# Kernel tuning notes

Hardware: AMD Instinct MI355X
Metric: run time of the kernel (lower is better)

## Reference

```python
import jax, jax.numpy as jnp
from jax import lax
import numpy as np

M, CLS, K, DL, DC, DO, BD = 87, 65, 128, 128, 128, 2048, 256
B, H, W = 256, 7, 7


def _c1(x, Wt, b):
    # 1x1 Conv2d: [B,Cin,H,W] -> [B,Cout,H,W]
    return jnp.einsum('oc,bchw->bohw', Wt, x) + b[None, :, None, None]


def _pagerank(edge, v_init, p=0.85, iters=100):
    # torch: transition = adj / adj.sum(dim=1)  (broadcast divides COLUMNS by row-sums)
    n = edge.shape[0]
    Wpr = p * edge / jnp.sum(edge, axis=1)[None, :]
    s = v_init * n                                  # [B,n,1]
    coef = (1.0 - p) / n
    def body(i, xv):
        zx = coef * jnp.sum(xv, axis=1, keepdims=True)      # z_T @ x -> [B,1,1]
        return jnp.einsum('ij,bjo->bio', Wpr, xv) + s * zx
    xv = lax.fori_loop(0, iters, body, s)
    nrm = jnp.sqrt(jnp.sum(xv * xv, axis=1, keepdims=True))  # F.normalize(dim=1)
    xv = xv / jnp.maximum(nrm, 1e-12)
    return (v_init + xv).reshape(v_init.shape[0], -1)        # [B,n]


def setup_inputs() -> dict:
    key = jax.random.key(0)
    ks = jax.random.split(key, 24)
    def w(k, shape, s=0.02):
        return jax.random.normal(k, shape, jnp.float32) * s
    rng = np.random.default_rng(0)
    A = (rng.random((M, M)) < 0.08).astype(np.float32)
    A = np.maximum(A, A.T)
    np.fill_diagonal(A, 1.0)   # symmetric adjacency with self-loops (degrees > 0)
    return {
        'x': jax.random.normal(ks[0], (B, DO, H, W), jnp.float32),
        'Wb': w(ks[1], (BD, DO)), 'bb': w(ks[2], (BD,), 0.01),
        'Wfc': w(ks[3], (CLS, BD)), 'Wfc2': w(ks[4], (CLS, BD)),
        'Wo1': w(ks[5], (4 * DL, DO)), 'bo1': w(ks[6], (4 * DL,), 0.01),
        'Wo2': w(ks[7], (DL, 4 * DL)), 'bo2': w(ks[8], (DL,), 0.01),
        'Wa': w(ks[9], (M, DL)), 'ba': w(ks[10], (M,), 0.01),
        'Wps': w(ks[11], (DC, DL)), 'bps': w(ks[12], (DC,), 0.01),
        'node_p': jax.random.uniform(ks[13], (K, M), jnp.float32, -0.1, 0.1),
        'Wg': w(ks[14], (DC, DC + K)), 'bg': w(ks[15], (DC,), 0.01),
        'Wsp': w(ks[16], (DL, DC)), 'bsp': w(ks[17], (DL,), 0.01),
        'Ws': w(ks[18], (1, DC + DL)), 'bs': w(ks[19], (1,), 0.01),
        'Wox1': w(ks[20], (4 * DL, DL)), 'box1': w(ks[21], (4 * DL,), 0.01),
        'Wox2': w(ks[22], (DO, 4 * DL)), 'box2': w(ks[23], (DO,), 0.01),
        'edge': jnp.asarray(A),
    }


def reference(x, Wb, bb, Wfc, Wfc2, Wo1, bo1, Wo2, bo2, Wa, ba, Wps, bps,
              node_p, Wg, bg, Wsp, bsp, Ws, bs, Wox1, box1, Wox2, box2, edge):
    Bsz, _, hl, wl = x.shape
    HW = hl * wl

    # global pooled branch
    x_p = jnp.mean(x, axis=(2, 3))                           # [B,2048]
    features_p = x_p @ Wb.T + bb                             # [B,256]
    pre_output = features_p @ Wfc.T                          # [B,65]
    pre_score = jax.nn.softmax(lax.stop_gradient(pre_output), axis=1)

    # personalized pagerank over the semantic graph (constant wrt grads)
    v_init = jnp.concatenate(
        [jnp.zeros((Bsz, M - CLS), x.dtype), pre_score], axis=1)[:, :, None]
    v_y = lax.stop_gradient(_pagerank(edge, v_init))         # [B,87]

    # local feature reduction 2048 -> 512 -> 128
    x_l = _c1(_c1(x, Wo1, bo1), Wo2, bo2)                    # [B,128,7,7]

    a = _c1(x_l, Wa, ba).reshape(Bsz, M, HW).transpose(0, 2, 1)   # [B,HW,87]
    ps = _c1(x_l, Wps, bps).reshape(Bsz, DC, HW)                  # [B,128,HW]
    m1 = jax.nn.relu(jnp.matmul(ps, a))                           # [B,128,87]

    # replicate torch's exact (k, B*m) reshape + flat v_y broadcast
    node = jnp.broadcast_to(node_p[None], (Bsz, K, M)).reshape(K, Bsz * M)
    node = (v_y.reshape(-1) * node).reshape(Bsz, K, M)

    g = jnp.einsum('oc,bcm->bom', Wg, jnp.concatenate([node, m1], axis=1)) \
        + bg[None, :, None]                                   # [B,128,87]

    # D^-1/2 A D^-1/2 graph propagation
    Dinv = jnp.sum(edge, axis=0) ** -0.5
    edge_norm = Dinv[:, None] * edge * Dinv[None, :]
    m2 = jax.nn.relu(jnp.einsum('bcm,mn->bcn', g, edge_norm))  # [B,128,87]

    sp = jnp.einsum('oc,bcm->bom', Wsp, m2) + bsp[None, :, None]  # [B,128,87]

    # conv_s over concat(m2_expand, x_expand) is separable: avoid the
    # [B,256,HW,87] tensor entirely (1 output channel, 1x1 kernel).
    Ws1, Ws2 = Ws[0, :DC], Ws[0, DC:]
    t_node = jnp.einsum('c,bcm->bm', Ws1, m2)                  # [B,87]
    t_pix = jnp.einsum('c,bcp->bp', Ws2, x_l.reshape(Bsz, DL, HW))  # [B,HW]
    s_logits = t_node[:, :, None] + t_pix[:, None, :] + bs[0]  # [B,87,HW]
    s_att = jax.nn.softmax(s_logits, axis=1)                   # softmax over nodes

    m3 = jax.nn.relu(jnp.matmul(sp, s_att)).reshape(Bsz, DL, hl, wl)
    m3 = _c1(_c1(m3, Wox1, box1), Wox2, box2)                  # [B,2048,7,7]

    feature_aug = jnp.mean(m3, axis=(2, 3)) @ Wb.T + bb
    features = features_p + feature_aug
    outputs2 = features @ Wfc2.T
    softmax_outputs = jax.nn.softmax(outputs2, axis=1)
    return (features, outputs2, softmax_outputs, pre_output, features_p)
```

## Files before the change

kernel.cpp:

```cpp
#include <hip/hip_runtime.h>
#include <cmath>


typedef __attribute__((ext_vector_type(8))) short short8;
typedef __attribute__((ext_vector_type(4))) short s16x4;
typedef __attribute__((ext_vector_type(4))) float f32x4;

constexpr size_t OFF_W12BF = 0;
constexpr size_t OFF_T1BF  = 131072;
constexpr size_t OFF_WBBF  = 262144;
constexpr size_t OFF_XPBF  = 524288;
constexpr size_t OFF_WAPBF = 786432;
constexpr size_t OFF_WG2BF = 800768;
constexpr size_t OFF_ENPBF = 808960;
constexpr size_t OFF_B215  = 813568;
constexpr size_t OFF_B12   = 813792;
constexpr size_t OFF_WPR   = 813920;
constexpr size_t OFF_BTMP  = 821496;
constexpr size_t OFF_WC    = 823544;
constexpr size_t OFF_BC    = 856312;
constexpr size_t OFF_VY    = 856568;
constexpr size_t OFF_NT    = 878848;
constexpr size_t OFF_PART  = 901376;

__device__ __forceinline__ unsigned short f2bf(float f) {
  unsigned u = __builtin_bit_cast(unsigned, f);
  u += 0x7fffu + ((u >> 16) & 1u);
  return (unsigned short)(u >> 16);
}
__device__ __forceinline__ float bf2f(unsigned short s) {
  return __builtin_bit_cast(float, ((unsigned)s) << 16);
}

__global__ __launch_bounds__(256) void ksetup_all(
    const float* __restrict__ Wb,  const float* __restrict__ bb,
    const float* __restrict__ Wa,  const float* __restrict__ ba,
    const float* __restrict__ Wps, const float* __restrict__ bps,
    const float* __restrict__ Wg,  const float* __restrict__ edge,
    const float* __restrict__ Wo2, const float* __restrict__ Wo1,
    const float* __restrict__ Wox2,const float* __restrict__ Wox1,
    const float* __restrict__ box1,const float* __restrict__ box2,
    const float* __restrict__ bo1, const float* __restrict__ bo2,
    float* __restrict__ ws, float* __restrict__ featp)
{
  __shared__ alignas(16) short As[64*72];
  __shared__ alignas(16) short Bs[64*72];
  int blk = blockIdx.x, tid = threadIdx.x;
  if (blk < 256) {
    int base = (blk*256 + tid)*8;
    float4 v0 = *(const float4*)&Wb[base];
    float4 v1 = *(const float4*)&Wb[base+4];
    short8 sv;
    sv[0]=(short)f2bf(v0.x); sv[1]=(short)f2bf(v0.y); sv[2]=(short)f2bf(v0.z); sv[3]=(short)f2bf(v0.w);
    sv[4]=(short)f2bf(v1.x); sv[5]=(short)f2bf(v1.y); sv[6]=(short)f2bf(v1.z); sv[7]=(short)f2bf(v1.w);
    *(short8*)&((unsigned short*)(ws+OFF_WBBF))[base] = sv;
  } else if (blk < 320) {
    int idx4 = ((blk-256)*256 + tid)*4;
    float4 bv = *(const float4*)&bb[idx4 & 255];
    *(float4*)&featp[idx4] = bv;
  } else if (blk < 352) {
    int idx4 = ((blk-320)*256 + tid)*4;
    float4 z; z.x=z.y=z.z=z.w=0.f;
    *(float4*)&ws[OFF_WC + idx4] = z;
  } else if (blk < 380) {
    int idx4 = ((blk-352)*256 + tid)*4;
    int r = idx4 >> 7, c = idx4 & 127;
    float4 v;
    if (r < 128)      v = *(const float4*)&Wps[r*128 + c];
    else if (r < 215) v = *(const float4*)&Wa[(r-128)*128 + c];
    else              { v.x=v.y=v.z=v.w=0.f; }
    s16x4 sv; sv[0]=(short)f2bf(v.x); sv[1]=(short)f2bf(v.y); sv[2]=(short)f2bf(v.z); sv[3]=(short)f2bf(v.w);
    *(s16x4*)&((unsigned short*)(ws+OFF_WAPBF))[idx4] = sv;
  } else if (blk < 396) {
    int idx4 = ((blk-380)*256 + tid)*4;
    int o = idx4 >> 7, d = idx4 & 127;
    float4 v = *(const float4*)&Wg[o*256 + 128 + d];
    s16x4 sv; sv[0]=(short)f2bf(v.x); sv[1]=(short)f2bf(v.y); sv[2]=(short)f2bf(v.z); sv[3]=(short)f2bf(v.w);
    *(s16x4*)&((unsigned short*)(ws+OFF_WG2BF))[idx4] = sv;
  } else if (blk < 432) {
    int idx = (blk-396)*256 + tid;
    int m = idx / 96, n = idx % 96;
    float v = 0.f;
    if (m < 87 && n < 87) {
      float sm = 0.f, sn = 0.f;
      for (int k = 0; k < 87; ++k) { sm += edge[k*87+m]; sn += edge[k*87+n]; }
      v = edge[m*87+n] / sqrtf(sm*sn);
    }
    ((unsigned short*)(ws+OFF_ENPBF))[idx] = f2bf(v);
  } else if (blk < 462) {
    int idx = (blk-432)*256 + tid;
    if (idx < 87*87) {
      int j = idx % 87;
      float rs = 0.f;
      for (int k = 0; k < 87; ++k) rs += edge[j*87+k];
      ws[OFF_WPR + idx] = 0.85f * edge[idx] / rs;
    }
  } else if (blk == 462) {
    if (tid < 224) {
      float v = (tid < 128) ? bps[tid] : (tid < 215 ? ba[tid-128] : 0.f);
      ws[OFF_B215 + tid] = v;
    }
  } else if (blk < 591) {
    int gb = blk - 463;
    const float *A, *B; unsigned short* C; int lda, ldb, ldc, i0, j0;
    if (gb < 64) {
      A = Wo2; B = Wo1; C = (unsigned short*)(ws+OFF_W12BF);
      lda = 512; ldb = 2048; ldc = 2048;
      i0 = (gb & 1)*64; j0 = (gb >> 1)*64;
    } else {
      int b2 = gb - 64;
      A = Wox2; B = Wox1; C = (unsigned short*)(ws+OFF_T1BF);
      lda = 512; ldb = 128; ldc = 128;
      i0 = (b2 >> 1)*64; j0 = (b2 & 1)*64;
    }
    int w = tid >> 6, l = tid & 63, quad = l >> 4, lane16 = l & 15;
    f32x4 acc[4];
    #pragma unroll
    for (int i = 0; i < 4; ++i) acc[i] = (f32x4)(0.f);
    for (int kc = 0; kc < 512; kc += 64) {
      for (int t = tid; t < 1024; t += 256) {
        int r = t >> 4, k4 = t & 15;
        float4 v = *(const float4*)&A[(size_t)(i0+r)*lda + kc + k4*4];
        s16x4 sv; sv[0]=(short)f2bf(v.x); sv[1]=(short)f2bf(v.y); sv[2]=(short)f2bf(v.z); sv[3]=(short)f2bf(v.w);
        *(s16x4*)&As[r*72 + k4*4] = sv;
      }
      for (int t = tid; t < 1024; t += 256) {
        int kr = t >> 4, n4 = t & 15;
        float4 v = *(const float4*)&B[(size_t)(kc+kr)*ldb + j0 + n4*4];
        Bs[(n4*4+0)*72 + kr] = (short)f2bf(v.x);
        Bs[(n4*4+1)*72 + kr] = (short)f2bf(v.y);
        Bs[(n4*4+2)*72 + kr] = (short)f2bf(v.z);
        Bs[(n4*4+3)*72 + kr] = (short)f2bf(v.w);
      }
      __syncthreads();
      #pragma unroll
      for (int ks = 0; ks < 2; ++ks) {
        short8 a = *(const short8*)&As[(w*16+lane16)*72 + ks*32 + quad*8];
        #pragma unroll
        for (int nt = 0; nt < 4; ++nt) {
          short8 b8 = *(const short8*)&Bs[(nt*16+lane16)*72 + ks*32 + quad*8];
          acc[nt] = __builtin_amdgcn_mfma_f32_16x16x32_bf16(a, b8, acc[nt], 0, 0, 0);
        }
      }
      __syncthreads();
    }
    #pragma unroll
    for (int nt = 0; nt < 4; ++nt)
      #pragma unroll
      for (int r = 0; r < 4; ++r)
        C[(size_t)(i0 + w*16 + quad*4 + r)*ldc + j0 + nt*16 + lane16] = f2bf(acc[nt][r]);
  } else {
    int vb = blk - 591;
    int w = tid >> 6, l = tid & 63;
    if (vb < 512) {
      int o = vb*4 + w;
      float s = 0.f;
      for (int h = l; h < 512; h += 64) s += Wox2[(size_t)o*512 + h] * box1[h];
      for (int off = 32; off; off >>= 1) s += __shfl_down(s, off, 64);
      if (l == 0) ws[OFF_BTMP + o] = s + box2[o];
    } else {
      int o = (vb - 512)*4 + w;
      float s = 0.f;
      for (int h = l; h < 512; h += 64) s += Wo2[(size_t)o*512 + h] * bo1[h];
      for (int off = 32; off; off >>= 1) s += __shfl_down(s, off, 64);
      if (l == 0) ws[OFF_B12 + o] = s + bo2[o];
    }
  }
}

__global__ __launch_bounds__(512, 4) void kmain5(const float* __restrict__ x,
                                                 const short* __restrict__ w12bf,
                                                 short* __restrict__ xpbf,
                                                 float* __restrict__ part)
{
  __shared__ alignas(16) short Bt[2][64*72];
  __shared__ alignas(16) float xpp[2][832];
  int b = blockIdx.x, q = blockIdx.y, tid = threadIdx.x;
  int w = tid >> 6, l = tid & 63;
  int quad = l >> 4, lane16 = l & 15;
  const float* xb = x + ((size_t)b*2048 + q*1024)*49;

  int p4A = tid % 13, cA = tid / 13;
  int tB = tid + 512;
  int p4B = tB % 13, cB = tB / 13;
  bool hasB = (tid < 320);

  float fA[4], fB[4];
  {
    if (p4A < 12) {
      float4 v = *(const float4*)(xb + cA*49 + p4A*4);
      fA[0]=v.x; fA[1]=v.y; fA[2]=v.z; fA[3]=v.w;
    } else fA[0] = xb[cA*49 + 48];
    if (hasB) {
      if (p4B < 12) {
        float4 v = *(const float4*)(xb + cB*49 + p4B*4);
        fB[0]=v.x; fB[1]=v.y; fB[2]=v.z; fB[3]=v.w;
      } else fB[0] = xb[cB*49 + 48];
    }
  }

  f32x4 acc[4];
  #pragma unroll
  for (int i = 0; i < 4; ++i) acc[i] = (f32x4)(0.f);

  for (int kci = 0; kci < 16; ++kci) {
    short* bt = Bt[kci & 1];
    float* xp = xpp[kci & 1];
    if (p4A < 12) {
      #pragma unroll
      for (int i = 0; i < 4; ++i) bt[(p4A*4+i)*72 + cA] = (short)f2bf(fA[i]);
      xp[tid] = fA[0]+fA[1]+fA[2]+fA[3];
    } else {
      bt[48*72 + cA] = (short)f2bf(fA[0]);
      xp[tid] = fA[0];
    }
    if (hasB) {
      if (p4B < 12) {
        #pragma unroll
        for (int i = 0; i < 4; ++i) bt[(p4B*4+i)*72 + cB] = (short)f2bf(fB[i]);
        xp[512 + tid] = fB[0]+fB[1]+fB[2]+fB[3];
      } else {
        bt[48*72 + cB] = (short)f2bf(fB[0]);
        xp[512 + tid] = fB[0];
      }
    }
    __syncthreads();
    if (kci < 15) {
      const float* xc = xb + (size_t)(kci+1)*64*49;
      if (p4A < 12) {
        float4 v = *(const float4*)(xc + cA*49 + p4A*4);
        fA[0]=v.x; fA[1]=v.y; fA[2]=v.z; fA[3]=v.w;
      } else fA[0] = xc[cA*49 + 48];
      if (hasB) {
        if (p4B < 12) {
          float4 v = *(const float4*)(xc + cB*49 + p4B*4);
          fB[0]=v.x; fB[1]=v.y; fB[2]=v.z; fB[3]=v.w;
        } else fB[0] = xc[cB*49 + 48];
      }
    }
    const short* wr = w12bf + (size_t)(w*16 + lane16)*2048 + q*1024 + kci*64 + quad*8;
    short8 a0 = *(const short8*)(wr);
    short8 a1 = *(const short8*)(wr + 32);
    #pragma unroll
    for (int ni = 0; ni < 4; ++ni) {
      const short* br = bt + (ni*16 + lane16)*72 + quad*8;
      short8 b0 = *(const short8*)(br);
      short8 b1 = *(const short8*)(br + 32);
      acc[ni] = __builtin_amdgcn_mfma_f32_16x16x32_bf16(a0, b0, acc[ni], 0, 0, 0);
      acc[ni] = __builtin_amdgcn_mfma_f32_16x16x32_bf16(a1, b1, acc[ni], 0, 0, 0);
    }
    if (tid < 64) {
      float s = 0.f;
      #pragma unroll
      for (int j = 0; j < 13; ++j) s += xp[tid*13 + j];
      xpbf[(size_t)b*2048 + q*1024 + kci*64 + tid] = (short)f2bf(s * (1.f/49.f));
    }
  }
  float* po = part + ((size_t)q*256 + b)*6656;
  #pragma unroll
  for (int ni = 0; ni < 4; ++ni) {
    int p = ni*16 + lane16;
    if (p < 49) {
      #pragma unroll
      for (int r = 0; r < 4; ++r) {
        int o = w*16 + quad*4 + r;
        po[o*52 + p] = acc[ni][r];
      }
    }
  }
}

__global__ __launch_bounds__(256) void kwcf(const float* __restrict__ Wb,
                                            const float* __restrict__ bb,
                                            const short* __restrict__ xpbf,
                                            float* __restrict__ featp,
                                            float* __restrict__ ws)
{
  __shared__ alignas(16) short As[64*72];
  __shared__ alignas(16) short Bs[64*72];
  int blk = blockIdx.x, tid = threadIdx.x;
  if (blk < 64) {
    const short* wbbf = (const short*)(ws+OFF_WBBF);
    const short* t1s  = (const short*)(ws+OFF_T1BF);
    int i0 = (blk & 3)*64, j0 = ((blk >> 2) & 1)*64, kc0 = (blk >> 3)*256;
    int w = tid >> 6, l = tid & 63, quad = l >> 4, lane16 = l & 15;
    f32x4 acc[4];
    #pragma unroll
    for (int i = 0; i < 4; ++i) acc[i] = (f32x4)(0.f);
    for (int kc = kc0; kc < kc0+256; kc += 64) {
      for (int t = tid; t < 512; t += 256) {
        int r = t >> 3, c8 = t & 7;
        *(short8*)&As[r*72 + c8*8] = *(const short8*)&wbbf[(size_t)(i0+r)*2048 + kc + c8*8];
      }
      for (int t = tid; t < 1024; t += 256) {
        int kr = t >> 4, n4 = t & 15;
        s16x4 v = *(const s16x4*)&t1s[(size_t)(kc+kr)*128 + j0 + n4*4];
        Bs[(n4*4+0)*72 + kr] = v[0];
        Bs[(n4*4+1)*72 + kr] = v[1];
        Bs[(n4*4+2)*72 + kr] = v[2];
        Bs[(n4*4+3)*72 + kr] = v[3];
      }
      __syncthreads();
      #pragma unroll
      for (int ks = 0; ks < 2; ++ks) {
        short8 a = *(const short8*)&As[(w*16+lane16)*72 + ks*32 + quad*8];
        #pragma unroll
        for (int nt = 0; nt < 4; ++nt) {
          short8 b8 = *(const short8*)&Bs[(nt*16+lane16)*72 + ks*32 + quad*8];
          acc[nt] = __builtin_amdgcn_mfma_f32_16x16x32_bf16(a, b8, acc[nt], 0, 0, 0);
        }
      }
      __syncthreads();
    }
    #pragma unroll
    for (int nt = 0; nt < 4; ++nt)
      #pragma unroll
      for (int r = 0; r < 4; ++r)
        atomicAdd(&ws[OFF_WC + (size_t)(i0 + w*16 + quad*4 + r)*128 + j0 + nt*16 + lane16], acc[nt][r]);
  } else if (blk < 128) {
    int j = (blk-64)*4 + (tid >> 6), l = tid & 63;
    float s = 0.f;
    for (int c = l; c < 2048; c += 64) s += Wb[(size_t)j*2048 + c] * ws[OFF_BTMP + c];
    for (int off = 32; off; off >>= 1) s += __shfl_down(s, off, 64);
    if (l == 0) ws[OFF_BC + j] = s + bb[j];
  } else {
    const short* wbbf = (const short*)(ws+OFF_WBBF);
    int idx = blk - 128;
    int i0 = (idx & 3)*64, j0 = ((idx >> 2) & 3)*64, kc0 = (idx >> 4)*256;
    int w = tid >> 6, l = tid & 63, quad = l >> 4, lane16 = l & 15;
    f32x4 acc[4];
    #pragma unroll
    for (int i = 0; i < 4; ++i) acc[i] = (f32x4)(0.f);
    for (int kc = kc0; kc < kc0+256; kc += 32) {
      short8 a = *(const short8*)&xpbf[(size_t)(i0 + w*16 + lane16)*2048 + kc + quad*8];
      #pragma unroll
      for (int nt = 0; nt < 4; ++nt) {
        short8 b8 = *(const short8*)&wbbf[(size_t)(j0 + nt*16 + lane16)*2048 + kc + quad*8];
        acc[nt] = __builtin_amdgcn_mfma_f32_16x16x32_bf16(a, b8, acc[nt], 0, 0, 0);
      }
    }
    #pragma unroll
    for (int nt = 0; nt < 4; ++nt)
      #pragma unroll
      for (int r = 0; r < 4; ++r)
        atomicAdd(&featp[(size_t)(i0 + w*16 + quad*4 + r)*256 + j0 + nt*16 + lane16], acc[nt][r]);
  }
}

__global__ __launch_bounds__(384) void kpr(const float* __restrict__ featp,
                                           const float* __restrict__ Wfc,
                                           const float* __restrict__ wpr,
                                           float* __restrict__ preo,
                                           float* __restrict__ vy)
{
  __shared__ alignas(16) float fpr[256];
  __shared__ alignas(16) float po[68];
  __shared__ alignas(16) float vsA[88];
  __shared__ alignas(16) float vsB[88];
  __shared__ alignas(16) float vis[88];
  __shared__ float rd[4];
  int b = blockIdx.x, tid = threadIdx.x;
  if (tid < 256) fpr[tid] = featp[b*256 + tid];
  __syncthreads();
  if (tid < 260) {
    int row = tid >> 2, p = tid & 3;
    float s = 0.f;
    const float* wr = Wfc + row*256 + p*64;
    #pragma unroll
    for (int c = 0; c < 64; c += 4) {
      float4 w4 = *(const float4*)&wr[c];
      s += w4.x*fpr[p*64+c] + w4.y*fpr[p*64+c+1] + w4.z*fpr[p*64+c+2] + w4.w*fpr[p*64+c+3];
    }
    s += __shfl_xor(s, 1, 64);
    s += __shfl_xor(s, 2, 64);
    if (p == 0) { po[row] = s; preo[b*65 + row] = s; }
  }
  __syncthreads();
  if (tid < 64) {
    float v = po[tid];
    if (tid == 0) v = fmaxf(v, po[64]);
    float mx = v;
    #pragma unroll
    for (int off = 32; off; off >>= 1) mx = fmaxf(mx, __shfl_down(mx, off, 64));
    mx = __shfl(mx, 0, 64);
    float e = expf(po[tid]-mx) + ((tid == 0) ? expf(po[64]-mx) : 0.f);
    float sm = e;
    #pragma unroll
    for (int off = 32; off; off >>= 1) sm += __shfl_down(sm, off, 64);
    if (tid == 0) { rd[0] = mx; rd[1] = 1.f/sm; }
  }
  __syncthreads();
  if (tid < 88) {
    float vin = (tid >= 22 && tid < 87) ? expf(po[tid-22]-rd[0])*rd[1] : 0.f;
    vis[tid] = vin;
    vsA[tid] = vin * 87.f;
    vsB[tid] = 0.f;
  }
  __syncthreads();
  float wrow[22];
  const int m4 = tid >> 2, pp = tid & 3;
  if (tid < 348) {
    float add = vis[m4] * 0.15f;
    #pragma unroll
    for (int jj = 0; jj < 22; ++jj) {
      int j = pp*22 + jj;
      wrow[jj] = (j < 87) ? (wpr[m4*87 + j] + add) : 0.f;
    }
  }
  for (int it = 0; it < 64; ++it) {
    const float* vc = (it & 1) ? vsB : vsA;
    float* vn = (it & 1) ? vsA : vsB;
    if (tid < 348) {
      float nv = 0.f;
      #pragma unroll
      for (int jj = 0; jj < 22; ++jj) nv += wrow[jj] * vc[pp*22 + jj];
      nv += __shfl_xor(nv, 1, 64);
      nv += __shfl_xor(nv, 2, 64);
      if (pp == 0) vn[m4] = nv;
    }
    __syncthreads();
  }
  if (tid < 64) {
    float v = vsA[tid]*vsA[tid];
    if (tid < 23) v += vsA[64+tid]*vsA[64+tid];
    #pragma unroll
    for (int off = 32; off; off >>= 1) v += __shfl_down(v, off, 64);
    if (tid == 0) rd[2] = 1.f / fmaxf(sqrtf(v), 1e-12f);
  }
  __syncthreads();
  if (tid < 87) vy[b*87 + tid] = vis[tid] + vsA[tid]*rd[2];
}

__global__ __launch_bounds__(384) void knode(const float* __restrict__ Wg,
                                             const float* __restrict__ node_p,
                                             const float* __restrict__ vy,
                                             float* __restrict__ nt)
{
  int tid = threadIdx.x;
  if (tid >= 352) return;
  int out = blockIdx.x*88 + (tid >> 2);
  int par = out / 11264;
  int r = out % 11264;
  int o = r / 88, m = r % 88;
  int p = tid & 3;
  float s = 0.f;
  if (m < 87) {
    const float* vrow = vy + (size_t)(par*128)*87 + m;
    for (int k = p*32; k < p*32+32; ++k)
      s += Wg[o*256 + k] * node_p[k*87 + m] * vrow[k*87];
  }
  s += __shfl_xor(s, 1, 64);
  s += __shfl_xor(s, 2, 64);
  if (p == 0) nt[out] = s;
}

__global__ __launch_bounds__(512) void kgraph_all(
    const float* __restrict__ part,  const float* __restrict__ b12,
    const short* __restrict__ wapbf, const float* __restrict__ b215,
    const short* __restrict__ wg2bf, const float* __restrict__ nt,
    const float* __restrict__ bg,    const short* __restrict__ enpbf,
    const float* __restrict__ Wsp,   const float* __restrict__ bsp,
    const float* __restrict__ Ws,    const float* __restrict__ wc,
    const float* __restrict__ bc,    const float* __restrict__ featp,
    const float* __restrict__ Wfc2,
    float* __restrict__ feat, float* __restrict__ out2, float* __restrict__ soft)
{
  extern __shared__ char smraw[];
  short* XT = (short*)smraw;
  short* At = XT + 8704;
  short* M1 = At + 16128;
  short* G  = M1 + 13056;
  short* M2 = G  + 13312;
  float* fb  = (float*)(M2 + 13312);
  float* wsm = fb;
  float* tnb = fb + 96;
  float* zs  = fb + 192;
  float* m3s = fb + 320;
  float* fs  = fb + 448;
  float* o2s = fb + 704;
  float* red = fb + 776;

  int b = blockIdx.x, tid = threadIdx.x;
  int w = tid >> 6, l = tid & 63, quad = l >> 4, lane16 = l & 15;

  const float* p0 = part + (size_t)b*6656;
  const float* p1 = p0 + (size_t)256*6656;
  for (int t = tid; t < 6656; t += 512) {
    int o = t / 52, p = t % 52;
    XT[p*136 + o] = (short)f2bf(p0[t] + p1[t] + b12[o]);
  }
  for (int t = tid; t < 1536; t += 512) {
    int p = 52 + t/128, o = t % 128;
    XT[p*136 + o] = 0;
  }
  __syncthreads();

  for (int t = w; t < 56; t += 8) {
    int mt = t >> 2, n4 = t & 3;
    f32x4 acc = (f32x4)(0.f);
    #pragma unroll
    for (int ks = 0; ks < 4; ++ks) {
      short8 a  = *(const short8*)&wapbf[(size_t)(mt*16+lane16)*128 + ks*32 + quad*8];
      short8 b8 = *(const short8*)&XT[(n4*16+lane16)*136 + ks*32 + quad*8];
      acc = __builtin_amdgcn_mfma_f32_16x16x32_bf16(a, b8, acc, 0, 0, 0);
    }
    int p = n4*16 + lane16;
    #pragma unroll
    for (int r = 0; r < 4; ++r) {
      int rr = mt*16 + quad*4 + r;
      At[rr*72 + p] = (p < 49) ? (short)f2bf(acc[r] + b215[rr]) : (short)0;
    }
  }
  __syncthreads();

  for (int t = w; t < 48; t += 8) {
    int mt = t / 8, n4 = t % 8;
    f32x4 acc = (f32x4)(0.f);
    #pragma unroll
    for (int ks = 0; ks < 2; ++ks) {
      short8 a  = *(const short8*)&At[(128 + mt*16 + lane16)*72 + ks*32 + quad*8];
      short8 b8 = *(const short8*)&At[(n4*16+lane16)*72 + ks*32 + quad*8];
      acc = __builtin_amdgcn_mfma_f32_16x16x32_bf16(a, b8, acc, 0, 0, 0);
    }
    int d = n4*16 + lane16;
    #pragma unroll
    for (int r = 0; r < 4; ++r) {
      int m = mt*16 + quad*4 + r;
      M1[m*136 + d] = (short)f2bf(fmaxf(acc[r], 0.f));
    }
  }
  __syncthreads();

  const float* ntb = nt + (size_t)(b & 1)*11264;
  for (int t = w; t < 48; t += 8) {
    int mt = t / 6, n4 = t % 6;
    f32x4 acc = (f32x4)(0.f);
    #pragma unroll
    for (int ks = 0; ks < 4; ++ks) {
      short8 a  = *(const short8*)&wg2bf[(size_t)(mt*16+lane16)*128 + ks*32 + quad*8];
      short8 b8 = *(const short8*)&M1[(n4*16+lane16)*136 + ks*32 + quad*8];
      acc = __builtin_amdgcn_mfma_f32_16x16x32_bf16(a, b8, acc, 0, 0, 0);
    }
    int m = n4*16 + lane16;
    #pragma unroll
    for (int r = 0; r < 4; ++r) {
      int o = mt*16 + quad*4 + r;
      float v = acc[r] + bg[o] + ((m < 88) ? ntb[o*88 + m] : 0.f);
      G[o*104 + m] = (short)f2bf(v);
    }
  }
  __syncthreads();

  for (int t = w; t < 48; t += 8) {
    int mt = t / 6, n4 = t % 6;
    f32x4 acc = (f32x4)(0.f);
    #pragma unroll
    for (int ks = 0; ks < 3; ++ks) {
      short8 a  = *(const short8*)&G[(mt*16+lane16)*104 + ks*32 + quad*8];
      short8 b8 = *(const short8*)&enpbf[(size_t)(n4*16+lane16)*96 + ks*32 + quad*8];
      acc = __builtin_amdgcn_mfma_f32_16x16x32_bf16(a, b8, acc, 0, 0, 0);
    }
    int n = n4*16 + lane16;
    #pragma unroll
    for (int r = 0; r < 4; ++r) {
      int c = mt*16 + quad*4 + r;
      M2[c*104 + n] = (short)f2bf(fmaxf(acc[r], 0.f));
    }
  }
  __syncthreads();

  if (tid < 348) {
    int m = tid >> 2, p = tid & 3;
    float s = 0.f;
    for (int c = p*32; c < p*32+32; ++c)
      s += Ws[c] * bf2f((unsigned short)M2[c*104 + m]);
    s += __shfl_xor(s, 1, 64);
    s += __shfl_xor(s, 2, 64);
    if (p == 0) tnb[m] = s;
  }
  __syncthreads();
  if (tid < 64) {
    float v = tnb[tid];
    if (tid < 23) v = fmaxf(v, tnb[64+tid]);
    float mx = v;
    #pragma unroll
    for (int off = 32; off; off >>= 1) mx = fmaxf(mx, __shfl_down(mx, off, 64));
    mx = __shfl(mx, 0, 64);
    float e0 = expf(tnb[tid]-mx);
    float e1 = (tid < 23) ? expf(tnb[64+tid]-mx) : 0.f;
    float sm = e0 + e1;
    #pragma unroll
    for (int off = 32; off; off >>= 1) sm += __shfl_down(sm, off, 64);
    sm = __shfl(sm, 0, 64);
    float inv = 1.f/sm;
    wsm[tid] = e0*inv;
    if (tid < 23) wsm[64+tid] = e1*inv;
  }
  __syncthreads();
  {
    int c = tid >> 2, p = tid & 3;
    float s = 0.f;
    for (int mm = p*22; mm < p*22+22 && mm < 87; ++mm)
      s += bf2f((unsigned short)M2[c*104 + mm]) * wsm[mm];
    s += __shfl_xor(s, 1, 64);
    s += __shfl_xor(s, 2, 64);
    if (p == 0) zs[c] = s;
  }
  __syncthreads();
  {
    int d = tid >> 2, p = tid & 3;
    float s = 0.f;
    for (int c = p*32; c < p*32+32; ++c) s += Wsp[d*128 + c] * zs[c];
    s += __shfl_xor(s, 1, 64);
    s += __shfl_xor(s, 2, 64);
    if (p == 0) m3s[d] = fmaxf(s + bsp[d], 0.f);
  }
  __syncthreads();

  if (tid < 256) {
    float s = 0.f;
    #pragma unroll 4
    for (int d4 = 0; d4 < 32; ++d4) {
      float4 w4 = *(const float4*)&wc[tid*128 + d4*4];
      s += w4.x*m3s[d4*4] + w4.y*m3s[d4*4+1] + w4.z*m3s[d4*4+2] + w4.w*m3s[d4*4+3];
    }
    float f = featp[b*256 + tid] + bc[tid] + s;
    fs[tid] = f;
    feat[b*256 + tid] = f;
  }
  __syncthreads();
  if (tid < 260) {
    int row = tid >> 2, p = tid & 3;
    float s = 0.f;
    for (int c = p*64; c < p*64+64; c += 4) {
      float4 w4 = *(const float4*)&Wfc2[row*256 + c];
      s += w4.x*fs[c] + w4.y*fs[c+1] + w4.z*fs[c+2] + w4.w*fs[c+3];
    }
    s += __shfl_xor(s, 1, 64);
    s += __shfl_xor(s, 2, 64);
    if (p == 0) { out2[b*65 + row] = s; o2s[row] = s; }
  }
  __syncthreads();
  if (tid < 64) {
    float v = o2s[tid];
    if (tid == 0) v = fmaxf(v, o2s[64]);
    float mx = v;
    #pragma unroll
    for (int off = 32; off; off >>= 1) mx = fmaxf(mx, __shfl_down(mx, off, 64));
    mx = __shfl(mx, 0, 64);
    float e = expf(o2s[tid]-mx) + ((tid == 0) ? expf(o2s[64]-mx) : 0.f);
    float sm = e;
    #pragma unroll
    for (int off = 32; off; off >>= 1) sm += __shfl_down(sm, off, 64);
    if (tid == 0) { red[0] = mx; red[1] = 1.f/sm; }
  }
  __syncthreads();
  if (tid < 65) soft[b*65 + tid] = expf(o2s[tid]-red[0]) * red[1];
}

extern "C" void kernel_launch(void* const* d_in, const int* in_sizes, int n_in,
                              void* d_out, int out_size, void* d_ws, size_t ws_size,
                              hipStream_t stream)
{
  (void)in_sizes; (void)n_in; (void)out_size; (void)ws_size;
  const float* x      = (const float*)d_in[0];
  const float* Wb     = (const float*)d_in[1];
  const float* bb     = (const float*)d_in[2];
  const float* Wfc    = (const float*)d_in[3];
  const float* Wfc2   = (const float*)d_in[4];
  const float* Wo1    = (const float*)d_in[5];
  const float* bo1    = (const float*)d_in[6];
  const float* Wo2    = (const float*)d_in[7];
  const float* bo2    = (const float*)d_in[8];
  const float* Wa     = (const float*)d_in[9];
  const float* ba     = (const float*)d_in[10];
  const float* Wps    = (const float*)d_in[11];
  const float* bps    = (const float*)d_in[12];
  const float* node_p = (const float*)d_in[13];
  const float* Wg     = (const float*)d_in[14];
  const float* bg     = (const float*)d_in[15];
  const float* Wsp    = (const float*)d_in[16];
  const float* bsp    = (const float*)d_in[17];
  const float* Ws     = (const float*)d_in[18];
  const float* Wox1   = (const float*)d_in[20];
  const float* box1   = (const float*)d_in[21];
  const float* Wox2   = (const float*)d_in[22];
  const float* box2   = (const float*)d_in[23];
  const float* edge   = (const float*)d_in[24];

  float* ws   = (float*)d_ws;
  float* out  = (float*)d_out;
  float* feat  = out;
  float* out2  = out + 65536;
  float* soft  = out + 82176;
  float* preo  = out + 98816;
  float* featp = out + 115456;

  ksetup_all<<<1135, 256, 0, stream>>>(Wb, bb, Wa, ba, Wps, bps, Wg, edge,
                                       Wo2, Wo1, Wox2, Wox1, box1, box2, bo1, bo2,
                                       ws, featp);
  kmain5<<<dim3(256,2), 512, 0, stream>>>(x, (const short*)(ws + OFF_W12BF),
                                          (short*)(ws + OFF_XPBF), ws + OFF_PART);
  kwcf<<<256, 256, 0, stream>>>(Wb, bb, (const short*)(ws + OFF_XPBF), featp, ws);
  kpr<<<256, 384, 0, stream>>>(featp, Wfc, ws + OFF_WPR, preo, ws + OFF_VY);
  knode<<<256, 384, 0, stream>>>(Wg, node_p, ws + OFF_VY, ws + OFF_NT);
  kgraph_all<<<256, 512, 132144, stream>>>(ws + OFF_PART, ws + OFF_B12,
                                           (const short*)(ws + OFF_WAPBF),
                                           ws + OFF_B215,
                                           (const short*)(ws + OFF_WG2BF),
                                           ws + OFF_NT, bg,
                                           (const short*)(ws + OFF_ENPBF),
                                           Wsp, bsp, Ws,
                                           ws + OFF_WC, ws + OFF_BC, featp, Wfc2,
                                           feat, out2, soft);
}
```

Measured before the change: 336.7 us.

## Split kmain5 reduction four ways and double-depth prefetch of x chunks

```diff
diff --git a/kernel.cpp b/kernel.cpp
--- a/kernel.cpp
+++ b/kernel.cpp
@@ -168,7 +168,37 @@
   }
 }
 
-__global__ __launch_bounds__(512, 4) void kmain5(const float* __restrict__ x,
+
+#define LOADCH(fR, gR, ptr) do {                                                  \
+    if (p4A < 12) { float4 v_ = *(const float4*)((ptr) + cA*49 + p4A*4);          \
+      fR[0]=v_.x; fR[1]=v_.y; fR[2]=v_.z; fR[3]=v_.w; }                           \
+    else fR[0] = (ptr)[cA*49 + 48];                                               \
+    if (hasB) {                                                                   \
+      if (p4B < 12) { float4 v_ = *(const float4*)((ptr) + cB*49 + p4B*4);        \
+        gR[0]=v_.x; gR[1]=v_.y; gR[2]=v_.z; gR[3]=v_.w; }                         \
+      else gR[0] = (ptr)[cB*49 + 48]; }                                           \
+  } while(0)
+
+#define STAGECH(fR, gR, bt, xp) do {                                              \
+    if (p4A < 12) {                                                               \
+      bt[(p4A*4+0)*72 + cA] = (short)f2bf(fR[0]);                                 \
+      bt[(p4A*4+1)*72 + cA] = (short)f2bf(fR[1]);                                 \
+      bt[(p4A*4+2)*72 + cA] = (short)f2bf(fR[2]);                                 \
+      bt[(p4A*4+3)*72 + cA] = (short)f2bf(fR[3]);                                 \
+      xp[tid] = fR[0]+fR[1]+fR[2]+fR[3];                                          \
+    } else { bt[48*72 + cA] = (short)f2bf(fR[0]); xp[tid] = fR[0]; }              \
+    if (hasB) {                                                                   \
+      if (p4B < 12) {                                                             \
+        bt[(p4B*4+0)*72 + cB] = (short)f2bf(gR[0]);                               \
+        bt[(p4B*4+1)*72 + cB] = (short)f2bf(gR[1]);                               \
+        bt[(p4B*4+2)*72 + cB] = (short)f2bf(gR[2]);                               \
+        bt[(p4B*4+3)*72 + cB] = (short)f2bf(gR[3]);                               \
+        xp[512 + tid] = gR[0]+gR[1]+gR[2]+gR[3];                                  \
+      } else { bt[48*72 + cB] = (short)f2bf(gR[0]); xp[512 + tid] = gR[0]; }      \
+    }                                                                             \
+  } while(0)
+
+__global__ __launch_bounds__(512, 6) void kmain5(const float* __restrict__ x,
                                                  const short* __restrict__ w12bf,
                                                  short* __restrict__ xpbf,
                                                  float* __restrict__ part)
@@ -178,67 +208,34 @@
   int b = blockIdx.x, q = blockIdx.y, tid = threadIdx.x;
   int w = tid >> 6, l = tid & 63;
   int quad = l >> 4, lane16 = l & 15;
-  const float* xb = x + ((size_t)b*2048 + q*1024)*49;
+  const float* xb = x + ((size_t)b*2048 + q*512)*49;
 
   int p4A = tid % 13, cA = tid / 13;
   int tB = tid + 512;
   int p4B = tB % 13, cB = tB / 13;
   bool hasB = (tid < 320);
 
-  float fA[4], fB[4];
-  {
-    if (p4A < 12) {
-      float4 v = *(const float4*)(xb + cA*49 + p4A*4);
-      fA[0]=v.x; fA[1]=v.y; fA[2]=v.z; fA[3]=v.w;
-    } else fA[0] = xb[cA*49 + 48];
-    if (hasB) {
-      if (p4B < 12) {
-        float4 v = *(const float4*)(xb + cB*49 + p4B*4);
-        fB[0]=v.x; fB[1]=v.y; fB[2]=v.z; fB[3]=v.w;
-      } else fB[0] = xb[cB*49 + 48];
-    }
-  }
+  float f0[4], g0[4], f1[4], g1[4];
+  LOADCH(f0, g0, xb);
+  LOADCH(f1, g1, xb + 64*49);
 
   f32x4 acc[4];
   #pragma unroll
   for (int i = 0; i < 4; ++i) acc[i] = (f32x4)(0.f);
 
-  for (int kci = 0; kci < 16; ++kci) {
+  #pragma unroll
+  for (int kci = 0; kci < 8; ++kci) {
     short* bt = Bt[kci & 1];
     float* xp = xpp[kci & 1];
-    if (p4A < 12) {
-      #pragma unroll
-      for (int i = 0; i < 4; ++i) bt[(p4A*4+i)*72 + cA] = (short)f2bf(fA[i]);
-      xp[tid] = fA[0]+fA[1]+fA[2]+fA[3];
-    } else {
-      bt[48*72 + cA] = (short)f2bf(fA[0]);
-      xp[tid] = fA[0];
-    }
-    if (hasB) {
-      if (p4B < 12) {
-        #pragma unroll
-        for (int i = 0; i < 4; ++i) bt[(p4B*4+i)*72 + cB] = (short)f2bf(fB[i]);
-        xp[512 + tid] = fB[0]+fB[1]+fB[2]+fB[3];
-      } else {
-        bt[48*72 + cB] = (short)f2bf(fB[0]);
-        xp[512 + tid] = fB[0];
-      }
-    }
+    if ((kci & 1) == 0) { STAGECH(f0, g0, bt, xp); }
+    else                { STAGECH(f1, g1, bt, xp); }
     __syncthreads();
-    if (kci < 15) {
-      const float* xc = xb + (size_t)(kci+1)*64*49;
-      if (p4A < 12) {
-        float4 v = *(const float4*)(xc + cA*49 + p4A*4);
-        fA[0]=v.x; fA[1]=v.y; fA[2]=v.z; fA[3]=v.w;
-      } else fA[0] = xc[cA*49 + 48];
-      if (hasB) {
-        if (p4B < 12) {
-          float4 v = *(const float4*)(xc + cB*49 + p4B*4);
-          fB[0]=v.x; fB[1]=v.y; fB[2]=v.z; fB[3]=v.w;
-        } else fB[0] = xc[cB*49 + 48];
-      }
-    }
-    const short* wr = w12bf + (size_t)(w*16 + lane16)*2048 + q*1024 + kci*64 + quad*8;
+    if (kci < 6) {
+      const float* xc = xb + (size_t)(kci+2)*64*49;
+      if ((kci & 1) == 0) { LOADCH(f0, g0, xc); }
+      else                { LOADCH(f1, g1, xc); }
+    }
+    const short* wr = w12bf + (size_t)(w*16 + lane16)*2048 + q*512 + kci*64 + quad*8;
     short8 a0 = *(const short8*)(wr);
     short8 a1 = *(const short8*)(wr + 32);
     #pragma unroll
@@ -253,7 +250,7 @@
       float s = 0.f;
       #pragma unroll
       for (int j = 0; j < 13; ++j) s += xp[tid*13 + j];
-      xpbf[(size_t)b*2048 + q*1024 + kci*64 + tid] = (short)f2bf(s * (1.f/49.f));
+      xpbf[(size_t)b*2048 + q*512 + kci*64 + tid] = (short)f2bf(s * (1.f/49.f));
     }
   }
   float* po = part + ((size_t)q*256 + b)*6656;
@@ -485,9 +482,11 @@
 
   const float* p0 = part + (size_t)b*6656;
   const float* p1 = p0 + (size_t)256*6656;
+  const float* p2 = p1 + (size_t)256*6656;
+  const float* p3 = p2 + (size_t)256*6656;
   for (int t = tid; t < 6656; t += 512) {
     int o = t / 52, p = t % 52;
-    XT[p*136 + o] = (short)f2bf(p0[t] + p1[t] + b12[o]);
+    XT[p*136 + o] = (short)f2bf(p0[t] + p1[t] + p2[t] + p3[t] + b12[o]);
   }
   for (int t = tid; t < 1536; t += 512) {
     int p = 52 + t/128, o = t % 128;
@@ -699,7 +698,7 @@
   ksetup_all<<<1135, 256, 0, stream>>>(Wb, bb, Wa, ba, Wps, bps, Wg, edge,
                                        Wo2, Wo1, Wox2, Wox1, box1, box2, bo1, bo2,
                                        ws, featp);
-  kmain5<<<dim3(256,2), 512, 0, stream>>>(x, (const short*)(ws + OFF_W12BF),
+  kmain5<<<dim3(256,4), 512, 0, stream>>>(x, (const short*)(ws + OFF_W12BF),
                                           (short*)(ws + OFF_XPBF), ws + OFF_PART);
   kwcf<<<256, 256, 0, stream>>>(Wb, bb, (const short*)(ws + OFF_XPBF), featp, ws);
   kpr<<<256, 384, 0, stream>>>(featp, Wfc, ws + OFF_WPR, preo, ws + OFF_VY);
```

After: 349.2 us. +3.7%, slower.

## Split main GEMM K four ways and prefetch setup GEMM tiles into registers

Applied to the files above, without the earlier changes.

```diff
diff --git a/kernel.cpp b/kernel.cpp
--- a/kernel.cpp
+++ b/kernel.cpp
@@ -114,25 +114,37 @@
       i0 = (b2 >> 1)*64; j0 = (b2 & 1)*64;
     }
     int w = tid >> 6, l = tid & 63, quad = l >> 4, lane16 = l & 15;
+    int rT[4], c4[4];
+    #pragma unroll
+    for (int j = 0; j < 4; ++j) { int t = tid + j*256; rT[j] = t >> 4; c4[j] = t & 15; }
+    float4 av[4], bv[4];
+    #pragma unroll
+    for (int j = 0; j < 4; ++j) {
+      av[j] = *(const float4*)&A[(size_t)(i0+rT[j])*lda + c4[j]*4];
+      bv[j] = *(const float4*)&B[(size_t)rT[j]*ldb + j0 + c4[j]*4];
+    }
     f32x4 acc[4];
     #pragma unroll
     for (int i = 0; i < 4; ++i) acc[i] = (f32x4)(0.f);
     for (int kc = 0; kc < 512; kc += 64) {
-      for (int t = tid; t < 1024; t += 256) {
-        int r = t >> 4, k4 = t & 15;
-        float4 v = *(const float4*)&A[(size_t)(i0+r)*lda + kc + k4*4];
-        s16x4 sv; sv[0]=(short)f2bf(v.x); sv[1]=(short)f2bf(v.y); sv[2]=(short)f2bf(v.z); sv[3]=(short)f2bf(v.w);
-        *(s16x4*)&As[r*72 + k4*4] = sv;
-      }
-      for (int t = tid; t < 1024; t += 256) {
-        int kr = t >> 4, n4 = t & 15;
-        float4 v = *(const float4*)&B[(size_t)(kc+kr)*ldb + j0 + n4*4];
-        Bs[(n4*4+0)*72 + kr] = (short)f2bf(v.x);
-        Bs[(n4*4+1)*72 + kr] = (short)f2bf(v.y);
-        Bs[(n4*4+2)*72 + kr] = (short)f2bf(v.z);
-        Bs[(n4*4+3)*72 + kr] = (short)f2bf(v.w);
+      #pragma unroll
+      for (int j = 0; j < 4; ++j) {
+        s16x4 sv; sv[0]=(short)f2bf(av[j].x); sv[1]=(short)f2bf(av[j].y);
+        sv[2]=(short)f2bf(av[j].z); sv[3]=(short)f2bf(av[j].w);
+        *(s16x4*)&As[rT[j]*72 + c4[j]*4] = sv;
+        Bs[(c4[j]*4+0)*72 + rT[j]] = (short)f2bf(bv[j].x);
+        Bs[(c4[j]*4+1)*72 + rT[j]] = (short)f2bf(bv[j].y);
+        Bs[(c4[j]*4+2)*72 + rT[j]] = (short)f2bf(bv[j].z);
+        Bs[(c4[j]*4+3)*72 + rT[j]] = (short)f2bf(bv[j].w);
       }
       __syncthreads();
+      if (kc < 448) {
+        #pragma unroll
+        for (int j = 0; j < 4; ++j) {
+          av[j] = *(const float4*)&A[(size_t)(i0+rT[j])*lda + (kc+64) + c4[j]*4];
+          bv[j] = *(const float4*)&B[(size_t)(kc+64+rT[j])*ldb + j0 + c4[j]*4];
+        }
+      }
       #pragma unroll
       for (int ks = 0; ks < 2; ++ks) {
         short8 a = *(const short8*)&As[(w*16+lane16)*72 + ks*32 + quad*8];
@@ -168,17 +180,16 @@
   }
 }
 
-__global__ __launch_bounds__(512, 4) void kmain5(const float* __restrict__ x,
+__global__ __launch_bounds__(512, 6) void kmain5(const float* __restrict__ x,
                                                  const short* __restrict__ w12bf,
                                                  short* __restrict__ xpbf,
                                                  float* __restrict__ part)
 {
   __shared__ alignas(16) short Bt[2][64*72];
-  __shared__ alignas(16) float xpp[2][832];
   int b = blockIdx.x, q = blockIdx.y, tid = threadIdx.x;
   int w = tid >> 6, l = tid & 63;
   int quad = l >> 4, lane16 = l & 15;
-  const float* xb = x + ((size_t)b*2048 + q*1024)*49;
+  const float* xb = x + ((size_t)b*2048 + q*512)*49;
 
   int p4A = tid % 13, cA = tid / 13;
   int tB = tid + 512;
@@ -203,29 +214,20 @@
   #pragma unroll
   for (int i = 0; i < 4; ++i) acc[i] = (f32x4)(0.f);
 
-  for (int kci = 0; kci < 16; ++kci) {
+  for (int kci = 0; kci < 8; ++kci) {
     short* bt = Bt[kci & 1];
-    float* xp = xpp[kci & 1];
     if (p4A < 12) {
       #pragma unroll
       for (int i = 0; i < 4; ++i) bt[(p4A*4+i)*72 + cA] = (short)f2bf(fA[i]);
-      xp[tid] = fA[0]+fA[1]+fA[2]+fA[3];
-    } else {
-      bt[48*72 + cA] = (short)f2bf(fA[0]);
-      xp[tid] = fA[0];
-    }
+    } else bt[48*72 + cA] = (short)f2bf(fA[0]);
     if (hasB) {
       if (p4B < 12) {
         #pragma unroll
         for (int i = 0; i < 4; ++i) bt[(p4B*4+i)*72 + cB] = (short)f2bf(fB[i]);
-        xp[512 + tid] = fB[0]+fB[1]+fB[2]+fB[3];
-      } else {
-        bt[48*72 + cB] = (short)f2bf(fB[0]);
-        xp[512 + tid] = fB[0];
-      }
+      } else bt[48*72 + cB] = (short)f2bf(fB[0]);
     }
     __syncthreads();
-    if (kci < 15) {
+    if (kci < 7) {
       const float* xc = xb + (size_t)(kci+1)*64*49;
       if (p4A < 12) {
         float4 v = *(const float4*)(xc + cA*49 + p4A*4);
@@ -238,7 +240,7 @@
         } else fB[0] = xc[cB*49 + 48];
       }
     }
-    const short* wr = w12bf + (size_t)(w*16 + lane16)*2048 + q*1024 + kci*64 + quad*8;
+    const short* wr = w12bf + (size_t)(w*16 + lane16)*2048 + q*512 + kci*64 + quad*8;
     short8 a0 = *(const short8*)(wr);
     short8 a1 = *(const short8*)(wr + 32);
     #pragma unroll
@@ -251,9 +253,9 @@
     }
     if (tid < 64) {
       float s = 0.f;
-      #pragma unroll
-      for (int j = 0; j < 13; ++j) s += xp[tid*13 + j];
-      xpbf[(size_t)b*2048 + q*1024 + kci*64 + tid] = (short)f2bf(s * (1.f/49.f));
+      for (int p = 0; p < 49; ++p)
+        s += bf2f((unsigned short)bt[p*72 + tid]);
+      xpbf[(size_t)b*2048 + q*512 + kci*64 + tid] = (short)f2bf(s * (1.f/49.f));
     }
   }
   float* po = part + ((size_t)q*256 + b)*6656;
@@ -485,9 +487,11 @@
 
   const float* p0 = part + (size_t)b*6656;
   const float* p1 = p0 + (size_t)256*6656;
+  const float* p2 = p1 + (size_t)256*6656;
+  const float* p3 = p2 + (size_t)256*6656;
   for (int t = tid; t < 6656; t += 512) {
     int o = t / 52, p = t % 52;
-    XT[p*136 + o] = (short)f2bf(p0[t] + p1[t] + b12[o]);
+    XT[p*136 + o] = (short)f2bf(p0[t] + p1[t] + p2[t] + p3[t] + b12[o]);
   }
   for (int t = tid; t < 1536; t += 512) {
     int p = 52 + t/128, o = t % 128;
@@ -699,7 +703,7 @@
   ksetup_all<<<1135, 256, 0, stream>>>(Wb, bb, Wa, ba, Wps, bps, Wg, edge,
                                        Wo2, Wo1, Wox2, Wox1, box1, box2, bo1, bo2,
                                        ws, featp);
-  kmain5<<<dim3(256,2), 512, 0, stream>>>(x, (const short*)(ws + OFF_W12BF),
+  kmain5<<<dim3(256,4), 512, 0, stream>>>(x, (const short*)(ws + OFF_W12BF),
                                           (short*)(ws + OFF_XPBF), ws + OFF_PART);
   kwcf<<<256, 256, 0, stream>>>(Wb, bb, (const short*)(ws + OFF_XPBF), featp, ws);
   kpr<<<256, 384, 0, stream>>>(featp, Wfc, ws + OFF_WPR, preo, ws + OFF_VY);
```

Result: faster. 315.0 us (-6.4%).
